# Performance work log

Measured on AMD Instinct MI355X. Metric: run time of the kernel, lower is better.

The kernel has to match this reference:

```python
import jax, jax.numpy as jnp
import numpy as np

NEG, NEG2, EPS, K = 0.01, 0.2, 1e-5, 10
B, N = 8, 2048

def lrelu(x, s):
    return jnp.where(x >= 0, x, s * x)

def bn_eval(x, g, b):
    # BatchNorm in eval mode with running_mean=0, running_var=1
    shp = [1] * x.ndim; shp[1] = -1
    return x * (g / np.sqrt(1.0 + EPS)).reshape(shp) + b.reshape(shp)

def conv1d(x, W, b):  # x [B,C,N], W [O,C]
    return jnp.einsum('bcn,oc->bon', x, W) + b[None, :, None]

def conv2d_1x1(x, W, b):  # x [B,C,N,K], W [O,C]
    return jnp.einsum('bcnk,oc->bonk', x, W) + b[None, :, None, None]

def edge_feats(x, k):
    # x: [B, d, N] -> [B, 2d, N, k]
    xt = jnp.swapaxes(x, 1, 2)                                   # [B,N,d]
    dist = (-2.0 * jnp.einsum('bnd,bdm->bnm', xt, x)
            + jnp.sum(xt ** 2, axis=2, keepdims=True)
            + jnp.sum(x ** 2, axis=1, keepdims=True))            # [B,N,N]
    idx = jnp.argsort(dist, axis=2)[:, :, 1:k + 1]               # [B,N,k]
    nbrs = jax.vmap(lambda xb, ib: xb[:, ib])(x, idx)            # [B,d,N,k]
    c = x[:, :, :, None]
    return jnp.concatenate([jnp.broadcast_to(c, nbrs.shape), nbrs - c], axis=1)

def edge_block(x, wc1, wcb1, bn1g, bn1b, wc2, wcb2, bn2g, bn2b,
               xc, xcb, xbng, xbnb, oW, ob):
    C = x.shape[1]
    ee = edge_feats(x, K)                                        # [B,2C,N,K]
    w = lrelu(bn_eval(conv2d_1x1(ee[:, C:], wc1, wcb1), bn1g, bn1b), NEG)
    w = lrelu(bn_eval(conv2d_1x1(w, wc2, wcb2), bn2g, bn2b), NEG)
    w = jax.nn.softmax(w, axis=-1)
    h = lrelu(bn_eval(conv2d_1x1(ee, xc, xcb), xbng, xbnb), NEG)
    # Conv2d(Fout, Fout, [1,K]): contract channels and neighbor axis
    return jnp.einsum('bcnj,ocj->bon', h * w, oW) + ob[None, :, None]

def adain(x, style, W, b):
    s = conv1d(style, W, b)
    g, be = jnp.split(s, 2, axis=1)
    m = jnp.mean(x, axis=2, keepdims=True)
    v = jnp.mean((x - m) ** 2, axis=2, keepdims=True)
    return g * ((x - m) * jax.lax.rsqrt(v + EPS)) + be

def _forward(z, x, hW1, hb1, hW2, hb2,
             e1_wc1, e1_wcb1, e1_bn1g, e1_bn1b, e1_wc2, e1_wcb2, e1_bn2g, e1_bn2b,
             e1_xc, e1_xcb, e1_xbng, e1_xbnb, e1_oW, e1_ob, a1_W, a1_b,
             e2_wc1, e2_wcb1, e2_bn1g, e2_bn1b, e2_wc2, e2_wcb2, e2_bn2g, e2_bn2b,
             e2_xc, e2_xcb, e2_xbng, e2_xbnb, e2_oW, e2_ob, a2_W, a2_b,
             gW1, gb1, gbn1g, gbn1b, gW2, gb2, gbn2g, gbn2b,
             tW1, tb1, tW2, tb2, tW3, tb3):
    st = jnp.swapaxes(jnp.concatenate([x, z], axis=-1), 1, 2)    # [B,3+nz,N]
    st = lrelu(conv1d(st, hW1, hb1), NEG)
    st = lrelu(conv1d(st, hW2, hb2), NEG)                        # [B,128,N]
    pc = jnp.swapaxes(x, 1, 2)                                   # [B,3,N]
    x1 = edge_block(pc, e1_wc1, e1_wcb1, e1_bn1g, e1_bn1b, e1_wc2, e1_wcb2,
                    e1_bn2g, e1_bn2b, e1_xc, e1_xcb, e1_xbng, e1_xbnb, e1_oW, e1_ob)
    x1 = adain(lrelu(x1, NEG2), st, a1_W, a1_b)                  # [B,64,N]
    x2 = edge_block(x1, e2_wc1, e2_wcb1, e2_bn1g, e2_bn1b, e2_wc2, e2_wcb2,
                    e2_bn2g, e2_bn2b, e2_xc, e2_xcb, e2_xbng, e2_xbnb, e2_oW, e2_ob)
    x2 = adain(lrelu(x2, NEG2), st, a2_W, a2_b)                  # [B,128,N]
    fg = jnp.max(x2, axis=2)                                     # [B,128]
    fg = lrelu(bn_eval(fg @ gW1.T + gb1, gbn1g, gbn1b), NEG)
    fg = lrelu(bn_eval(fg @ gW2.T + gb2, gbn2g, gbn2b), NEG)     # [B,512]
    fg = jnp.broadcast_to(fg[:, :, None], (fg.shape[0], 512, x2.shape[2]))
    feat = jnp.concatenate([fg, x2], axis=1)                     # [B,640,N]
    t = lrelu(conv1d(feat, tW1, tb1), NEG)
    t = lrelu(conv1d(t, tW2, tb2), NEG)
    t = conv1d(t, tW3, tb3)
    return jnp.swapaxes(t, 1, 2)                                 # [B,N,3]

_PARAM_SPECS = [
    ('hW1', (128, 131)), ('hb1', (128,)), ('hW2', (128, 128)), ('hb2', (128,)),
    ('e1_wc1', (32, 3)), ('e1_wcb1', (32,)), ('e1_bn1g', (32,)), ('e1_bn1b', (32,)),
    ('e1_wc2', (64, 32)), ('e1_wcb2', (64,)), ('e1_bn2g', (64,)), ('e1_bn2b', (64,)),
    ('e1_xc', (64, 6)), ('e1_xcb', (64,)), ('e1_xbng', (64,)), ('e1_xbnb', (64,)),
    ('e1_oW', (64, 64, 10)), ('e1_ob', (64,)), ('a1_W', (128, 128)), ('a1_b', (128,)),
    ('e2_wc1', (64, 64)), ('e2_wcb1', (64,)), ('e2_bn1g', (64,)), ('e2_bn1b', (64,)),
    ('e2_wc2', (128, 64)), ('e2_wcb2', (128,)), ('e2_bn2g', (128,)), ('e2_bn2b', (128,)),
    ('e2_xc', (128, 128)), ('e2_xcb', (128,)), ('e2_xbng', (128,)), ('e2_xbnb', (128,)),
    ('e2_oW', (128, 128, 10)), ('e2_ob', (128,)), ('a2_W', (256, 128)), ('a2_b', (256,)),
    ('gW1', (128, 128)), ('gb1', (128,)), ('gbn1g', (128,)), ('gbn1b', (128,)),
    ('gW2', (512, 128)), ('gb2', (512,)), ('gbn2g', (512,)), ('gbn2b', (512,)),
    ('tW1', (256, 640)), ('tb1', (256,)), ('tW2', (64, 256)), ('tb2', (64,)),
    ('tW3', (3, 64)), ('tb3', (3,)),
]

def setup_inputs() -> dict:
    key = jax.random.key(0)
    d = {
        'z': jax.random.normal(jax.random.fold_in(key, 1000), (B, N, 128), jnp.float32),
        'x': jax.random.normal(jax.random.fold_in(key, 1001), (B, N, 3), jnp.float32),
    }
    for i, (nm, sh) in enumerate(_PARAM_SPECS):
        v = 0.1 * jax.random.normal(jax.random.fold_in(key, i), sh, jnp.float32)
        if nm.endswith('g'):  # batchnorm gammas around 1
            v = v + 1.0
        d[nm] = v
    return d

def reference(z, x, hW1, hb1, hW2, hb2,
              e1_wc1, e1_wcb1, e1_bn1g, e1_bn1b, e1_wc2, e1_wcb2, e1_bn2g, e1_bn2b,
              e1_xc, e1_xcb, e1_xbng, e1_xbnb, e1_oW, e1_ob, a1_W, a1_b,
              e2_wc1, e2_wcb1, e2_bn1g, e2_bn1b, e2_wc2, e2_wcb2, e2_bn2g, e2_bn2b,
              e2_xc, e2_xcb, e2_xbng, e2_xbnb, e2_oW, e2_ob, a2_W, a2_b,
              gW1, gb1, gbn1g, gbn1b, gW2, gb2, gbn2g, gbn2b,
              tW1, tb1, tW2, tb2, tW3, tb3):
    return _forward(z, x, hW1, hb1, hW2, hb2,
                    e1_wc1, e1_wcb1, e1_bn1g, e1_bn1b, e1_wc2, e1_wcb2, e1_bn2g, e1_bn2b,
                    e1_xc, e1_xcb, e1_xbng, e1_xbnb, e1_oW, e1_ob, a1_W, a1_b,
                    e2_wc1, e2_wcb1, e2_bn1g, e2_bn1b, e2_wc2, e2_wcb2, e2_bn2g, e2_bn2b,
                    e2_xc, e2_xcb, e2_xbng, e2_xbnb, e2_oW, e2_ob, a2_W, a2_b,
                    gW1, gb1, gbn1g, gbn1b, gW2, gb2, gbn2g, gbn2b,
                    tW1, tb1, tW2, tb2, tW3, tb3)
```

## Files before the change

### kernel.cpp

```cpp
#include <hip/hip_runtime.h>
#include <math.h>

#define NPTS 2048
#define BATCH 8
#define KNB 10
#define NT (NPTS*KNB)

static __device__ __forceinline__ float lrelu(float x, float s){ return x >= 0.f ? x : s*x; }
static __device__ __forceinline__ double lrelu_d(double x, double s){ return x >= 0.0 ? x : s*x; }

template<int TM, int TN>
__global__ __launch_bounds__(256) void gemm_bn(
    const float* __restrict__ In, int ldn, size_t inBS, int koff,
    const float* __restrict__ W, int wstride, int wcol0,
    const float* __restrict__ cb, const float* __restrict__ bng, const float* __restrict__ bnb,
    const float* __restrict__ addBO, int addM,
    float* __restrict__ Out, int ldo, size_t outBS,
    int C, int act, float neg, int bbase)
{
  constexpr int RM = TM/16, RN = TN/16;
  __shared__ float As[16][TM+4];
  __shared__ float Bs[16][TN+4];
  const int b = bbase + blockIdx.z;
  const float* in = In + (size_t)b*inBS;
  float* outp = Out + (size_t)b*outBS;
  const int m0 = blockIdx.y*TM, n0 = blockIdx.x*TN;
  const int t = threadIdx.x;
  const int tmv = t>>4, tnv = t&15;
  float acc[RM][RN] = {};
  for (int k0=0; k0<C; k0+=16){
    #pragma unroll
    for (int s=0;s<RM;s++){
      const int i = t + s*256;
      const int k = i&15, m = i>>4;
      As[k][m] = W[(size_t)(m0+m)*wstride + wcol0 + k0 + k];
    }
    #pragma unroll
    for (int s=0;s<RN;s++){
      const int i = t + s*256;
      const int n = i & (TN-1), kk2 = i / TN;
      Bs[kk2][n] = in[(size_t)(koff + k0 + kk2)*ldn + n0 + n];
    }
    __syncthreads();
    #pragma unroll
    for (int kk=0;kk<16;kk++){
      float av[RM], bv[RN];
      #pragma unroll
      for (int s=0;s<RM/4;s++){
        float4 v = *(const float4*)&As[kk][tmv*RM + s*4];
        av[s*4]=v.x; av[s*4+1]=v.y; av[s*4+2]=v.z; av[s*4+3]=v.w;
      }
      #pragma unroll
      for (int s=0;s<RN/4;s++){
        float4 v = *(const float4*)&Bs[kk][tnv*RN + s*4];
        bv[s*4]=v.x; bv[s*4+1]=v.y; bv[s*4+2]=v.z; bv[s*4+3]=v.w;
      }
      #pragma unroll
      for (int i2=0;i2<RM;i2++)
        #pragma unroll
        for (int j2=0;j2<RN;j2++) acc[i2][j2] += av[i2]*bv[j2];
    }
    __syncthreads();
  }
  const float rs = 1.f/sqrtf(1.f + 1e-5f);
  #pragma unroll
  for (int i2=0;i2<RM;i2++){
    const int gm = m0 + tmv*RM + i2;
    float addv = cb ? cb[gm] : 0.f;
    if (addBO) addv += addBO[b*addM + gm];
    float sc = 1.f, bs = 0.f;
    if (bng){ sc = bng[gm]*rs; bs = bnb[gm]; }
    float* orow = outp + (size_t)gm*ldo + n0 + tnv*RN;
    #pragma unroll
    for (int j4=0;j4<RN/4;j4++){
      float4 o;
      float vv[4];
      #pragma unroll
      for (int q=0;q<4;q++){
        float v = acc[i2][j4*4+q] + addv;
        if (bng) v = v*sc + bs;
        if (act) v = lrelu(v, neg);
        vv[q] = v;
      }
      o.x=vv[0]; o.y=vv[1]; o.z=vv[2]; o.w=vv[3];
      *(float4*)&orow[j4*4] = o;
    }
  }
}

__global__ __launch_bounds__(256) void conv_gemm_exact(
    const float* __restrict__ in, const float* __restrict__ W, int wstride, int wcol0,
    const float* __restrict__ bias,
    float* __restrict__ out, int C, int M, int act, float neg)
{
  __shared__ float As[16][68];
  __shared__ float Bs[16][68];
  const int b = blockIdx.z;
  const int m0 = blockIdx.y*64, n0 = blockIdx.x*64;
  const int t = threadIdx.x;
  const int tm = t>>4, tn = t&15;
  float acc[4][4] = {};
  for (int k0 = 0; k0 < C; k0 += 16){
    #pragma unroll
    for (int i=0;i<4;i++){
      const int ii = t + i*256;
      const int k = ii&15, m = ii>>4;
      const int gm = m0+m, gk = k0+k;
      As[k][m] = (gm<M && gk<C) ? W[(size_t)gm*wstride + wcol0 + gk] : 0.f;
    }
    #pragma unroll
    for (int i=0;i<4;i++){
      const int ii = t + i*256;
      const int n = ii&63, k = ii>>6;
      const int gk = k0+k;
      Bs[k][n] = (gk<C) ? in[((size_t)b*C+gk)*NPTS + n0+n] : 0.f;
    }
    __syncthreads();
    #pragma unroll
    for (int k=0;k<16;k++){
      #pragma unroll
      for (int i=0;i<4;i++){
        const float a = As[k][tm*4+i];
        #pragma unroll
        for (int j=0;j<4;j++){
          acc[i][j] = __fadd_rn(acc[i][j], __fmul_rn(a, Bs[k][tn*4+j]));
        }
      }
    }
    __syncthreads();
  }
  #pragma unroll
  for (int i=0;i<4;i++){
    const int gm = m0 + tm*4 + i;
    if (gm < M){
      const float bv = bias ? bias[gm] : 0.f;
      #pragma unroll
      for (int j=0;j<4;j++){
        float v = __fadd_rn(acc[i][j], bv);
        if (act) v = (v >= 0.f) ? v : __fmul_rn(neg, v);
        out[((size_t)b*M+gm)*NPTS + n0 + tn*4 + j] = v;
      }
    }
  }
}

__global__ __launch_bounds__(256) void head1_exact(
    const float* __restrict__ x, const float* __restrict__ z,
    const float* __restrict__ W, const float* __restrict__ bias,
    float* __restrict__ outh)
{
  __shared__ float As[16][68];
  __shared__ float Bs[16][68];
  const int b = blockIdx.z;
  const int m0 = blockIdx.y*64, n0 = blockIdx.x*64;
  const int t = threadIdx.x;
  const int tm = t>>4, tn = t&15;
  float acc[4][4] = {};
  for (int k0 = 0; k0 < 144; k0 += 16){
    #pragma unroll
    for (int i=0;i<4;i++){
      const int ii = t + i*256;
      const int k = ii&15, m = ii>>4;
      const int gk = k0+k;
      As[k][m] = (gk<131) ? W[(size_t)(m0+m)*131 + gk] : 0.f;
    }
    #pragma unroll
    for (int i=0;i<4;i++){
      const int ii = t + i*256;
      const int k = ii&15, nn = ii>>4;
      const int gk = k0+k, gn = n0+nn;
      float v = 0.f;
      if (gk < 3)        v = x[((size_t)b*NPTS+gn)*3   + gk];
      else if (gk < 131) v = z[((size_t)b*NPTS+gn)*128 + (gk-3)];
      Bs[k][nn] = v;
    }
    __syncthreads();
    #pragma unroll
    for (int k=0;k<16;k++){
      #pragma unroll
      for (int i=0;i<4;i++){
        const float a = As[k][tm*4+i];
        #pragma unroll
        for (int j=0;j<4;j++){
          acc[i][j] = __fadd_rn(acc[i][j], __fmul_rn(a, Bs[k][tn*4+j]));
        }
      }
    }
    __syncthreads();
  }
  #pragma unroll
  for (int i=0;i<4;i++){
    const int gm = m0 + tm*4 + i;
    #pragma unroll
    for (int j=0;j<4;j++){
      float v = __fadd_rn(acc[i][j], bias[gm]);
      v = (v >= 0.f) ? v : __fmul_rn(0.01f, v);
      outh[((size_t)b*128+gm)*NPTS + n0 + tn*4 + j] = v;
    }
  }
}

__global__ __launch_bounds__(256) void norms3_f32(const float* __restrict__ Xn, float* __restrict__ XN)
{
  const int q = blockIdx.x*256 + threadIdx.x;
  const float* p = Xn + (size_t)q*3;
  float s = __fmul_rn(p[0],p[0]);
  s = __fadd_rn(s, __fmul_rn(p[1],p[1]));
  s = __fadd_rn(s, __fmul_rn(p[2],p[2]));
  XN[q] = s;
}

__global__ __launch_bounds__(256) void knn_part3(
    const float* __restrict__ Xn, const float* __restrict__ XN,
    double* __restrict__ topd, int* __restrict__ topi)
{
  const int t = threadIdx.x;
  const int qloc = t & 31, part = t >> 5;
  const int q = blockIdx.x*32 + qloc;
  const int b = q >> 11, n = q & (NPTS-1);
  const float* xb = Xn + (size_t)b*NPTS*3;
  const float qx = xb[(size_t)n*3+0], qy = xb[(size_t)n*3+1], qz = xb[(size_t)n*3+2];
  const float qn = XN[q];
  float td[11]; int ti[11];
  #pragma unroll
  for (int r=0;r<11;r++){ td[r] = 3.4e38f; ti[r] = 0x7fffffff; }
  const int m0 = part*(NPTS/8);
  for (int mm=0; mm<NPTS/8; mm++){
    const int m = m0 + mm;
    float dot = __fmul_rn(qx, xb[(size_t)m*3+0]);
    dot = __fadd_rn(dot, __fmul_rn(qy, xb[(size_t)m*3+1]));
    dot = __fadd_rn(dot, __fmul_rn(qz, xb[(size_t)m*3+2]));
    float dist = __fmul_rn(-2.f, dot);
    dist = __fadd_rn(dist, qn);
    dist = __fadd_rn(dist, XN[b*NPTS + m]);
    if (dist < td[10]){
      td[10] = dist; ti[10] = m;
      #pragma unroll
      for (int p=10;p>0;p--){
        if (td[p] < td[p-1]){
          float tf=td[p]; td[p]=td[p-1]; td[p-1]=tf;
          int   tt=ti[p]; ti[p]=ti[p-1]; ti[p-1]=tt;
        }
      }
    }
  }
  const size_t base = ((size_t)q*8 + part)*11;
  #pragma unroll
  for (int r=0;r<11;r++){ topd[base+r] = (double)td[r]; topi[base+r] = ti[r]; }
}

__global__ __launch_bounds__(256) void knn_merge_kernel(
    const double* __restrict__ topd, const int* __restrict__ topi, int* __restrict__ idxout)
{
  const int q = blockIdx.x*256 + threadIdx.x;
  double td[11]; int ti[11];
  #pragma unroll
  for (int r=0;r<11;r++){ td[r] = 1.0e308; ti[r] = 0x7fffffff; }
  const size_t base = (size_t)q*88;
  for (int s=0; s<88; s++){
    const double d = topd[base+s];
    const int  im = topi[base+s];
    if (d < td[10] || (d == td[10] && im < ti[10])){
      td[10] = d; ti[10] = im;
      #pragma unroll
      for (int p=10;p>0;p--){
        const bool sw = (td[p] < td[p-1]) || (td[p] == td[p-1] && ti[p] < ti[p-1]);
        if (sw){
          double tf=td[p]; td[p]=td[p-1]; td[p-1]=tf;
          int    tt=ti[p]; ti[p]=ti[p-1]; ti[p-1]=tt;
        }
      }
    }
  }
  #pragma unroll
  for (int j=0;j<KNB;j++) idxout[(size_t)q*KNB + j] = ti[j+1];
}

__global__ __launch_bounds__(256) void norms64_f32(const float* __restrict__ Xn, float* __restrict__ XN)
{
  const int q = blockIdx.x*256 + threadIdx.x;
  const float4* p4 = (const float4*)(Xn + (size_t)q*64);
  float s0=0.f,s1=0.f,s2=0.f,s3=0.f;
  #pragma unroll
  for (int d4=0; d4<16; d4++){
    float4 v = p4[d4];
    s0 += v.x*v.x; s1 += v.y*v.y; s2 += v.z*v.z; s3 += v.w*v.w;
  }
  XN[q] = (s0+s1)+(s2+s3);
}

__global__ __launch_bounds__(256) void knn_coarse(
    const float* __restrict__ Xn, const float* __restrict__ XN,
    float* __restrict__ topf, int* __restrict__ topi)
{
  __shared__ float Cs[64][68];
  __shared__ float xns[64];
  const int t = threadIdx.x;
  const int tq = t>>3, p = t&7;
  const int q0 = blockIdx.x*32;
  const int b  = q0 >> 11;
  const int gq = q0 + tq;
  const int nloc = (q0 & (NPTS-1)) + tq;
  const float* xb = Xn + (size_t)b*NPTS*64;
  float qv[64];
  {
    const float4* p4 = (const float4*)(xb + (size_t)nloc*64);
    #pragma unroll
    for (int d4=0; d4<16; d4++){ float4 v = p4[d4]; qv[d4*4]=v.x; qv[d4*4+1]=v.y; qv[d4*4+2]=v.z; qv[d4*4+3]=v.w; }
  }
  const float qn = XN[gq];
  float td[16]; int ti[16];
  #pragma unroll
  for (int r=0;r<16;r++){ td[r] = 3.4e38f; ti[r] = 0x7fffffff; }

  for (int m0=0; m0<NPTS; m0+=64){
    __syncthreads();
    #pragma unroll
    for (int s=0;s<4;s++){
      const int i = t + s*256;
      const int row = i>>4, f4 = i&15;
      float4 v = *(const float4*)(xb + (size_t)(m0+row)*64 + f4*4);
      *(float4*)&Cs[row][f4*4] = v;
    }
    if (t < 64) xns[t] = XN[b*NPTS + m0 + t];
    __syncthreads();
    #pragma unroll
    for (int jj=0;jj<8;jj++){
      const int row = jj*8 + p;
      float d0=0.f,d1=0.f,d2=0.f,d3=0.f;
      #pragma unroll
      for (int k4=0;k4<16;k4++){
        float4 v = *(const float4*)&Cs[row][k4*4];
        d0 += qv[k4*4+0]*v.x; d1 += qv[k4*4+1]*v.y;
        d2 += qv[k4*4+2]*v.z; d3 += qv[k4*4+3]*v.w;
      }
      const float dist = qn - 2.f*((d0+d1)+(d2+d3)) + xns[row];
      const int m = m0 + row;
      if (dist < td[15]){
        td[15] = dist; ti[15] = m;
        #pragma unroll
        for (int pp=15;pp>0;pp--){
          if (td[pp] < td[pp-1]){
            float tf=td[pp]; td[pp]=td[pp-1]; td[pp-1]=tf;
            int   tt=ti[pp]; ti[pp]=ti[pp-1]; ti[pp-1]=tt;
          }
        }
      }
    }
  }
  const size_t base = ((size_t)gq*8 + p)*16;
  #pragma unroll
  for (int r=0;r<16;r++){ topf[base+r] = td[r]; topi[base+r] = ti[r]; }
}

__global__ __launch_bounds__(256) void norms64d(const double* __restrict__ Xn, double* __restrict__ XN)
{
  const int q = blockIdx.x*256 + threadIdx.x;
  const double* p = Xn + (size_t)q*64;
  double s = 0.0;
  #pragma unroll
  for (int d=0; d<64; d++) s += p[d]*p[d];
  XN[q] = s;
}

__global__ __launch_bounds__(256) void knn_refine(
    const float* __restrict__ topf, const int* __restrict__ topi,
    const double* __restrict__ Xd, const double* __restrict__ XNd,
    int* __restrict__ idxout)
{
  const int q = blockIdx.x*256 + threadIdx.x;
  const int b = q >> 11;
  float tf[16]; int ti[16];
  #pragma unroll
  for (int r=0;r<16;r++){ tf[r] = 3.4e38f; ti[r] = 0x7fffffff; }
  const size_t base = (size_t)q*128;
  for (int s=0; s<128; s++){
    const float d = topf[base+s];
    const int  im = topi[base+s];
    if (d < tf[15] || (d == tf[15] && im < ti[15])){
      tf[15] = d; ti[15] = im;
      #pragma unroll
      for (int p=15;p>0;p--){
        const bool sw = (tf[p] < tf[p-1]) || (tf[p] == tf[p-1] && ti[p] < ti[p-1]);
        if (sw){
          float a=tf[p]; tf[p]=tf[p-1]; tf[p-1]=a;
          int   c=ti[p]; ti[p]=ti[p-1]; ti[p-1]=c;
        }
      }
    }
  }
  double qv[64];
  {
    const double2* p2 = (const double2*)(Xd + (size_t)q*64);
    #pragma unroll
    for (int d2=0; d2<32; d2++){ double2 v = p2[d2]; qv[d2*2]=v.x; qv[d2*2+1]=v.y; }
  }
  const double qn = XNd[q];
  double dd[11]; int di[11];
  #pragma unroll
  for (int r=0;r<11;r++){ dd[r] = 1.0e308; di[r] = 0x7fffffff; }
  for (int s=0; s<16; s++){
    const int m = ti[s];
    const double2* c2 = (const double2*)(Xd + ((size_t)(b*NPTS + m))*64);
    double d0=0.0,d1=0.0,d2s=0.0,d3=0.0;
    #pragma unroll
    for (int d4=0; d4<16; d4++){
      double2 va = c2[d4*2], vb = c2[d4*2+1];
      d0 += qv[d4*4+0]*va.x; d1 += qv[d4*4+1]*va.y;
      d2s+= qv[d4*4+2]*vb.x; d3 += qv[d4*4+3]*vb.y;
    }
    const double dot = (d0+d1)+(d2s+d3);
    const double dist = (qn - 2.0*dot) + XNd[b*NPTS + m];
    if (dist < dd[10] || (dist == dd[10] && m < di[10])){
      dd[10] = dist; di[10] = m;
      #pragma unroll
      for (int p=10;p>0;p--){
        const bool sw = (dd[p] < dd[p-1]) || (dd[p] == dd[p-1] && di[p] < di[p-1]);
        if (sw){
          double a=dd[p]; dd[p]=dd[p-1]; dd[p-1]=a;
          int    c=di[p]; di[p]=di[p-1]; di[p-1]=c;
        }
      }
    }
  }
  #pragma unroll
  for (int j=0;j<KNB;j++) idxout[(size_t)q*KNB + j] = di[j+1];
}

__global__ __launch_bounds__(512) void edge1_f64(
    const float* __restrict__ Xn, const int* __restrict__ idx,
    const float* __restrict__ wc1, const float* __restrict__ wcb1,
    const float* __restrict__ bn1g, const float* __restrict__ bn1b,
    const float* __restrict__ wc2, const float* __restrict__ wcb2,
    const float* __restrict__ bn2g, const float* __restrict__ bn2b,
    const float* __restrict__ xc,  const float* __restrict__ xcb,
    const float* __restrict__ xbng, const float* __restrict__ xbnb,
    const float* __restrict__ oWT, const float* __restrict__ ob,
    double* __restrict__ outX)
{
  __shared__ float wc1s[32][3];
  __shared__ float wc2s[64][33];
  __shared__ float xcs[64][7];
  __shared__ float wcb1s[32], wcb2s[64], xcbs[64];
  __shared__ double fs1d[32], fb1d[32], fs2d[64], fb2d[64], fsxd[64], fbxd[64];
  __shared__ float cenb[8][3], difb[8][3];
  __shared__ double w1bd[8][32];
  __shared__ float smw2[4096];
  __shared__ double hwbd[8][64];

  const int t = threadIdx.x;
  const double sq = sqrt(1.0 + 1e-5);
  for (int i=t; i<96;   i+=512) wc1s[i/3][i%3] = wc1[i];
  for (int i=t; i<2048; i+=512) wc2s[i/32][i%32] = wc2[i];
  for (int i=t; i<384;  i+=512) xcs[i/6][i%6] = xc[i];
  if (t < 32){ wcb1s[t]=wcb1[t]; fs1d[t]=(double)bn1g[t]/sq; fb1d[t]=(double)bn1b[t]; }
  else if (t < 96){ int o=t-32; wcb2s[o]=wcb2[o]; fs2d[o]=(double)bn2g[o]/sq; fb2d[o]=(double)bn2b[o]; }
  else if (t < 160){ int o=t-96; xcbs[o]=xcb[o]; fsxd[o]=(double)xbng[o]/sq; fbxd[o]=(double)xbnb[o]; }
  __syncthreads();

  const int wid = t>>6, lane = t&63;
  const int p = blockIdx.x*8 + wid;
  const int b = p >> 11, n = p & (NPTS-1);
  const float* xb = Xn + (size_t)b*NPTS*3;
  if (lane < 3) cenb[wid][lane] = xb[(size_t)n*3 + lane];
  __builtin_amdgcn_wave_barrier();
  const int* ip = idx + ((size_t)b*NPTS + n)*KNB;

  double w2r[KNB], hr[KNB];
  #pragma unroll
  for (int j=0;j<KNB;j++){
    const int id = ip[j];
    if (lane < 3) difb[wid][lane] = __fadd_rn(xb[(size_t)id*3 + lane], -cenb[wid][lane]);
    __builtin_amdgcn_wave_barrier();
    if (lane < 32){
      float s = __fmul_rn(wc1s[lane][0], difb[wid][0]);
      s = __fadd_rn(s, __fmul_rn(wc1s[lane][1], difb[wid][1]));
      s = __fadd_rn(s, __fmul_rn(wc1s[lane][2], difb[wid][2]));
      s = __fadd_rn(s, wcb1s[lane]);
      const double y = (double)s * fs1d[lane] + fb1d[lane];
      w1bd[wid][lane] = lrelu_d(y, 0.01);
    }
    __builtin_amdgcn_wave_barrier();
    {
      const int o = lane;
      double s2 = 0.0;
      #pragma unroll 8
      for (int m=0;m<32;m++) s2 += (double)wc2s[o][m] * w1bd[wid][m];
      s2 += (double)wcb2s[o];
      w2r[j] = lrelu_d(s2*fs2d[o] + fb2d[o], 0.01);
      float s3 = __fmul_rn(xcs[o][0], cenb[wid][0]);
      s3 = __fadd_rn(s3, __fmul_rn(xcs[o][1], cenb[wid][1]));
      s3 = __fadd_rn(s3, __fmul_rn(xcs[o][2], cenb[wid][2]));
      s3 = __fadd_rn(s3, __fmul_rn(xcs[o][3], difb[wid][0]));
      s3 = __fadd_rn(s3, __fmul_rn(xcs[o][4], difb[wid][1]));
      s3 = __fadd_rn(s3, __fmul_rn(xcs[o][5], difb[wid][2]));
      s3 = __fadd_rn(s3, xcbs[o]);
      hr[j] = lrelu_d((double)s3*fsxd[o] + fbxd[o], 0.01);
    }
    __builtin_amdgcn_wave_barrier();
  }

  double hw[KNB];
  {
    double mx = w2r[0];
    #pragma unroll
    for (int j=1;j<KNB;j++) mx = fmax(mx, w2r[j]);
    double ssum = 0.0;
    #pragma unroll
    for (int j=0;j<KNB;j++){ const double e = exp(w2r[j]-mx); w2r[j]=e; ssum+=e; }
    #pragma unroll
    for (int j=0;j<KNB;j++) hw[j] = hr[j]*(w2r[j]/ssum);
  }

  double acc = 0.0;
  #pragma unroll
  for (int j=0;j<KNB;j++){
    __syncthreads();
    for (int i=t; i<4096; i+=512) smw2[i] = oWT[(size_t)j*4096 + i];
    hwbd[wid][lane] = hw[j];
    __syncthreads();
    double s = 0.0;
    #pragma unroll 8
    for (int c=0;c<64;c++) s += (double)smw2[c*64 + lane]*hwbd[wid][c];
    acc += s;
  }
  outX[((size_t)b*64+lane)*NPTS + n] = acc + (double)ob[lane];
}

template<int CH>
__global__ void owt_kernel(const float* __restrict__ oW, float* __restrict__ oWT)
{
  const int i = blockIdx.x*256 + threadIdx.x;
  if (i < CH*CH*KNB){
    const int j  = i % KNB;
    const int c2 = (i / KNB) % CH;
    const int o  = i / (KNB*CH);
    oWT[((size_t)j*CH + c2)*CH + o] = oW[i];
  }
}

__global__ __launch_bounds__(256) void adain1_f64(
    double* __restrict__ X, const float* __restrict__ S)
{
  const int c = blockIdx.x, b = blockIdx.y;
  const int t = threadIdx.x;
  const size_t base = ((size_t)b*64 + c)*NPTS;
  __shared__ double red[256];
  double v[8];
  double s = 0.0;
  #pragma unroll
  for (int i=0;i<8;i++){
    double xv = X[base + t + i*256];
    xv = lrelu_d(xv, 0.2);
    v[i] = xv; s += xv;
  }
  red[t] = s; __syncthreads();
  for (int st=128; st>0; st>>=1){ if (t<st) red[t] += red[t+st]; __syncthreads(); }
  const double mean = red[0]/(double)NPTS;
  __syncthreads();
  double s2 = 0.0;
  #pragma unroll
  for (int i=0;i<8;i++){ const double d = v[i]-mean; s2 += d*d; }
  red[t] = s2; __syncthreads();
  for (int st=128; st>0; st>>=1){ if (t<st) red[t] += red[t+st]; __syncthreads(); }
  const double var  = red[0]/(double)NPTS;
  const double rstd = 1.0/sqrt(var + 1e-5);
  const float* g  = S + ((size_t)b*128 + c)*NPTS;
  const float* be = S + ((size_t)b*128 + 64 + c)*NPTS;
  #pragma unroll
  for (int i=0;i<8;i++){
    const int n = t + i*256;
    X[base+n] = (double)g[n]*((v[i]-mean)*rstd) + (double)be[n];
  }
}

__global__ __launch_bounds__(256) void transpose_cast64(
    const double* __restrict__ in, double* __restrict__ outT,
    float* __restrict__ outTf, float* __restrict__ outC)
{
  __shared__ double tile[64][65];
  const int b = blockIdx.y, n0 = blockIdx.x*64;
  const int t = threadIdx.x;
  for (int i=t; i<4096; i+=256){
    const int n=i&63, c=i>>6;
    const double v = in[((size_t)b*64+c)*NPTS + n0+n];
    tile[c][n] = v;
    outC[((size_t)b*64+c)*NPTS + n0+n] = (float)v;
  }
  __syncthreads();
  for (int i=t; i<4096; i+=256){
    const int c=i&63, n=i>>6;
    const double v = tile[c][n];
    outT [((size_t)b*NPTS+n0+n)*64 + c] = v;
    outTf[((size_t)b*NPTS+n0+n)*64 + c] = (float)v;
  }
}

__global__ __launch_bounds__(256) void kernelP(
    const float* __restrict__ x1c, const float* __restrict__ wc1,
    const float* __restrict__ xc,
    float* __restrict__ WCC, float* __restrict__ HCC)
{
  __shared__ float As[16][68];
  __shared__ float Bs[16][132];
  const int b = blockIdx.z;
  const int y = blockIdx.y;
  const int n0 = blockIdx.x*128;
  const int t = threadIdx.x;
  const int tm = t>>4, tn = t&15;
  float acc[4][8] = {};
  for (int k0=0; k0<64; k0+=16){
    #pragma unroll
    for (int s=0;s<4;s++){
      const int i = t + s*256;
      const int k = i&15, m = i>>4;
      float w;
      if (y == 0) w = wc1[(size_t)m*64 + k0 + k];
      else {
        const int c = (y-1)*64 + m;
        w = xc[(size_t)c*128 + k0 + k] - xc[(size_t)c*128 + 64 + k0 + k];
      }
      As[k][m] = w;
    }
    #pragma unroll
    for (int s=0;s<8;s++){
      const int i = t + s*256;
      const int n = i&127, kk = i>>7;
      Bs[kk][n] = x1c[((size_t)b*64 + k0 + kk)*NPTS + n0 + n];
    }
    __syncthreads();
    #pragma unroll
    for (int k=0;k<16;k++){
      float4 a4 = *(const float4*)&As[k][tm*4];
      const float av[4] = {a4.x, a4.y, a4.z, a4.w};
      #pragma unroll
      for (int j=0;j<8;j++){
        const float bv = Bs[k][tn + j*16];
        #pragma unroll
        for (int i2=0;i2<4;i2++) acc[i2][j] += av[i2]*bv;
      }
    }
    __syncthreads();
  }
  #pragma unroll
  for (int i2=0;i2<4;i2++){
    const int m = tm*4 + i2;
    #pragma unroll
    for (int j=0;j<8;j++){
      const int n = n0 + tn + j*16;
      if (y == 0) WCC[((size_t)b*64 + m)*NPTS + n] = acc[i2][j];
      else        HCC[((size_t)b*128 + (y-1)*64 + m)*NPTS + n] = acc[i2][j];
    }
  }
}

__global__ __launch_bounds__(256) void kernelA(
    const float* __restrict__ X1f, const int* __restrict__ IDX,
    const float* __restrict__ WCC,
    const float* __restrict__ wc1, const float* __restrict__ wcb1,
    const float* __restrict__ bn1g, const float* __restrict__ bn1b,
    float* __restrict__ W1, int bbase)
{
  __shared__ float wc1T[64*68];
  __shared__ float nbr[64*132];
  __shared__ int idx_l[128];
  const int b = bbase + blockIdx.z;
  const int n0 = blockIdx.x*128;
  const int t = threadIdx.x;
  const float* xb = X1f + (size_t)b*NPTS*64;

  if (t < 128){
    const int n = n0 + t;
    idx_l[t] = IDX[((size_t)b*NPTS + n/10)*KNB + (n%10)];
  }
  for (int i=t; i<4096; i+=256){
    const int k = i&63, m = i>>6;
    wc1T[k*68 + m] = wc1[(size_t)m*64 + k];
  }
  __syncthreads();
  const float4* xb4 = (const float4*)xb;
  #pragma unroll
  for (int r=0; r<8; r++){
    const int i = t + r*256;
    const int pos = i>>4, q4 = i&15;
    const float4 v = xb4[(size_t)idx_l[pos]*16 + q4];
    nbr[(q4*4+0)*132 + pos] = v.x;
    nbr[(q4*4+1)*132 + pos] = v.y;
    nbr[(q4*4+2)*132 + pos] = v.z;
    nbr[(q4*4+3)*132 + pos] = v.w;
  }
  __syncthreads();

  const int tm = t>>4, tn = t&15;
  float acc[4][8] = {};
  #pragma unroll 4
  for (int k=0;k<64;k++){
    float4 a4 = *(const float4*)&wc1T[k*68 + tm*4];
    const float av[4] = {a4.x, a4.y, a4.z, a4.w};
    #pragma unroll
    for (int j=0;j<8;j++){
      const float bv = nbr[k*132 + tn + j*16];
      #pragma unroll
      for (int i2=0;i2<4;i2++) acc[i2][j] += av[i2]*bv;
    }
  }
  const float rs = 1.f/sqrtf(1.f + 1e-5f);
  #pragma unroll
  for (int i2=0;i2<4;i2++){
    const int m = tm*4 + i2;
    const float bias = wcb1[m];
    const float sc = bn1g[m]*rs, bb = bn1b[m];
    #pragma unroll
    for (int j=0;j<8;j++){
      const int n = n0 + tn + j*16;
      const int p = n/10;
      float v = acc[i2][j] - WCC[((size_t)b*64 + m)*NPTS + p] + bias;
      v = lrelu(v*sc + bb, 0.01f);
      W1[((size_t)(b-bbase)*64 + m)*NT + n] = v;
    }
  }
}

#define C_WC2T 0
#define C_XCDT 4352
#define C_W1S  8704
#define C_NBRS 13952
#define C_TOT  19200
#define C_HW   0
#define C_OWL  5184

__global__ __launch_bounds__(256) void kernelC(
    const float* __restrict__ X1f, const int* __restrict__ IDX,
    const float* __restrict__ W1, const float* __restrict__ HCC,
    const float* __restrict__ wc2, const float* __restrict__ wcb2,
    const float* __restrict__ bn2g, const float* __restrict__ bn2b,
    const float* __restrict__ xc,  const float* __restrict__ xcb,
    const float* __restrict__ xbng, const float* __restrict__ xbnb,
    const float* __restrict__ oW, const float* __restrict__ ob,
    float* __restrict__ X2, int bbase)
{
  __shared__ float smC[C_TOT];
  __shared__ int idxC[80];
  const int b = bbase + blockIdx.z;
  const int n0 = blockIdx.x*80;
  const int p0 = n0/10;
  const int t = threadIdx.x;
  const float* xb = X1f + (size_t)b*NPTS*64;

  if (t < 80){
    const int n = n0 + t;
    idxC[t] = IDX[((size_t)b*NPTS + n/10)*KNB + (n%10)];
  }
  __syncthreads();

  const int tmv = t>>4, tnv = t&15, tnv5 = tnv*5;
  const int p_loc = tnv>>1, jh5 = (tnv&1)*5;
  const int o = t&127, phalf = t>>7;
  const float rs = 1.f/sqrtf(1.f + 1e-5f);
  float acc2[4] = {};

  for (int ch=0; ch<2; ch++){
    for (int i=t; i<4096; i+=256){
      const int k = i&63, cl = i>>6;
      smC[C_WC2T + k*68 + cl] = wc2[(size_t)(ch*64+cl)*64 + k];
      smC[C_XCDT + k*68 + cl] = xc[(size_t)(ch*64+cl)*128 + 64 + k];
    }
    for (int i=t; i<5120; i+=256){
      const int n = i%80, k = i/80;
      smC[C_W1S + k*82 + n] = W1[((size_t)(b-bbase)*64 + k)*NT + n0 + n];
    }
    {
      const float4* xb4 = (const float4*)xb;
      #pragma unroll
      for (int r=0;r<5;r++){
        const int i = t + r*256;
        const int pos = i>>4, q4 = i&15;
        const float4 v = xb4[(size_t)idxC[pos]*16 + q4];
        smC[C_NBRS + (q4*4+0)*82 + pos] = v.x;
        smC[C_NBRS + (q4*4+1)*82 + pos] = v.y;
        smC[C_NBRS + (q4*4+2)*82 + pos] = v.z;
        smC[C_NBRS + (q4*4+3)*82 + pos] = v.w;
      }
    }
    __syncthreads();

    float accw[4][5] = {}, acch[4][5] = {};
    #pragma unroll 2
    for (int k=0;k<64;k++){
      float4 a4 = *(const float4*)&smC[C_WC2T + k*68 + tmv*4];
      float4 x4 = *(const float4*)&smC[C_XCDT + k*68 + tmv*4];
      const float av[4] = {a4.x,a4.y,a4.z,a4.w};
      const float xv[4] = {x4.x,x4.y,x4.z,x4.w};
      float bw[5], bh[5];
      #pragma unroll
      for (int j=0;j<5;j++){
        bw[j] = smC[C_W1S  + k*82 + tnv5 + j];
        bh[j] = smC[C_NBRS + k*82 + tnv5 + j];
      }
      #pragma unroll
      for (int i2=0;i2<4;i2++)
        #pragma unroll
        for (int j=0;j<5;j++){ accw[i2][j]+=av[i2]*bw[j]; acch[i2][j]+=xv[i2]*bh[j]; }
    }

    float hwreg[4][5];
    #pragma unroll
    for (int i2=0;i2<4;i2++){
      const int c = ch*64 + tmv*4 + i2;
      const float s2 = bn2g[c]*rs, b2 = bn2b[c], cb2 = wcb2[c];
      const float sx = xbng[c]*rs, bx = xbnb[c], cbx = xcb[c];
      const float hcc = HCC[((size_t)b*128 + c)*NPTS + p0 + p_loc];
      float w2[5], hv[5];
      #pragma unroll
      for (int j=0;j<5;j++){
        w2[j] = lrelu((accw[i2][j] + cb2)*s2 + b2, 0.01f);
        hv[j] = lrelu((acch[i2][j] + hcc + cbx)*sx + bx, 0.01f);
      }
      float mx = w2[0];
      #pragma unroll
      for (int j=1;j<5;j++) mx = fmaxf(mx, w2[j]);
      mx = fmaxf(mx, __shfl_xor(mx, 1));
      float ssum = 0.f;
      #pragma unroll
      for (int j=0;j<5;j++){ w2[j] = expf(w2[j]-mx); ssum += w2[j]; }
      ssum += __shfl_xor(ssum, 1);
      const float inv = 1.f/ssum;
      #pragma unroll
      for (int j=0;j<5;j++) hwreg[i2][j] = hv[j]*(w2[j]*inv);
    }
    __syncthreads();

    #pragma unroll
    for (int i2=0;i2<4;i2++){
      const int cl = tmv*4 + i2;
      #pragma unroll
      for (int j=0;j<5;j++)
        smC[C_HW + p_loc*648 + cl*10 + jh5 + j] = hwreg[i2][j];
    }
    __syncthreads();

    for (int kc=0; kc<640; kc+=64){
      #pragma unroll
      for (int r=0;r<32;r++){
        const int i = t + r*256;
        const int oo = i>>6, kk = i&63;
        smC[C_OWL + oo*65 + kk] = oW[(size_t)oo*1280 + ch*640 + kc + kk];
      }
      __syncthreads();
      #pragma unroll 4
      for (int kk=0; kk<64; kk+=4){
        const float w0 = smC[C_OWL + o*65 + kk];
        const float w1v= smC[C_OWL + o*65 + kk+1];
        const float w2v= smC[C_OWL + o*65 + kk+2];
        const float w3v= smC[C_OWL + o*65 + kk+3];
        #pragma unroll
        for (int pp=0;pp<4;pp++){
          const float4 h4 = *(const float4*)&smC[C_HW + (phalf*4+pp)*648 + kc + kk];
          acc2[pp] += w0*h4.x + w1v*h4.y + w2v*h4.z + w3v*h4.w;
        }
      }
      __syncthreads();
    }
  }
  const float obv = ob[o];
  #pragma unroll
  for (int pp=0;pp<4;pp++)
    X2[((size_t)b*128 + o)*NPTS + p0 + phalf*4 + pp] = acc2[pp] + obv;
}

template<int CH>
__global__ __launch_bounds__(256) void adain_kernel(
    float* __restrict__ X, const float* __restrict__ S)
{
  const int c = blockIdx.x, b = blockIdx.y;
  const int t = threadIdx.x;
  const size_t base = ((size_t)b*CH + c)*NPTS;
  __shared__ float red[256];
  float v[8];
  float s = 0.f;
  #pragma unroll
  for (int i=0;i<8;i++){
    float xv = X[base + t + i*256];
    xv = lrelu(xv, 0.2f);
    v[i] = xv; s += xv;
  }
  red[t] = s; __syncthreads();
  for (int st=128; st>0; st>>=1){ if (t<st) red[t] += red[t+st]; __syncthreads(); }
  const float mean = red[0]*(1.f/NPTS);
  __syncthreads();
  float s2 = 0.f;
  #pragma unroll
  for (int i=0;i<8;i++){ const float d = v[i]-mean; s2 += d*d; }
  red[t] = s2; __syncthreads();
  for (int st=128; st>0; st>>=1){ if (t<st) red[t] += red[t+st]; __syncthreads(); }
  const float var  = red[0]*(1.f/NPTS);
  const float rstd = 1.f/sqrtf(var + 1e-5f);
  const float* g  = S + ((size_t)b*2*CH + c)*NPTS;
  const float* be = S + ((size_t)b*2*CH + CH + c)*NPTS;
  #pragma unroll
  for (int i=0;i<8;i++){
    const int n = t + i*256;
    X[base+n] = g[n]*((v[i]-mean)*rstd) + be[n];
  }
}

__global__ __launch_bounds__(256) void maxn_kernel(const float* __restrict__ X, float* __restrict__ FG)
{
  const int c = blockIdx.x, b = blockIdx.y;
  const int t = threadIdx.x;
  const float* p = X + ((size_t)b*128 + c)*NPTS;
  __shared__ float red[256];
  float m = -3.4e38f;
  for (int i=t; i<NPTS; i+=256) m = fmaxf(m, p[i]);
  red[t] = m; __syncthreads();
  for (int st=128; st>0; st>>=1){ if (t<st) red[t] = fmaxf(red[t], red[t+st]); __syncthreads(); }
  if (t == 0) FG[b*128+c] = red[0];
}

__global__ __launch_bounds__(512) void fc_kernel(
    const float* __restrict__ FG,
    const float* __restrict__ gW1, const float* __restrict__ gb1,
    const float* __restrict__ gbn1g, const float* __restrict__ gbn1b,
    const float* __restrict__ gW2, const float* __restrict__ gb2,
    const float* __restrict__ gbn2g, const float* __restrict__ gbn2b,
    const float* __restrict__ tW1, const float* __restrict__ tb1,
    float* __restrict__ FGP)
{
  const int b = blockIdx.x, t = threadIdx.x;
  __shared__ float fg[128], h1[128], h2[512];
  const float rs = 1.f/sqrtf(1.f + 1e-5f);
  if (t < 128) fg[t] = FG[b*128+t];
  __syncthreads();
  if (t < 128){
    float s = 0.f;
    for (int c=0;c<128;c++) s += gW1[t*128+c]*fg[c];
    s += gb1[t];
    s = s*(gbn1g[t]*rs) + gbn1b[t];
    h1[t] = lrelu(s, 0.01f);
  }
  __syncthreads();
  {
    float s = 0.f;
    for (int c=0;c<128;c++) s += gW2[t*128+c]*h1[c];
    s += gb2[t];
    s = s*(gbn2g[t]*rs) + gbn2b[t];
    h2[t] = lrelu(s, 0.01f);
  }
  __syncthreads();
  if (t < 256){
    float s = tb1[t];
    for (int c=0;c<512;c++) s += tW1[(size_t)t*640 + c]*h2[c];
    FGP[b*256+t] = s;
  }
}

__global__ __launch_bounds__(256) void t3_kernel(
    const float* __restrict__ T2, const float* __restrict__ tW3,
    const float* __restrict__ tb3, float* __restrict__ outp)
{
  __shared__ float w[192];
  const int t = threadIdx.x;
  if (t < 192) w[t] = tW3[t];
  __syncthreads();
  const int b = blockIdx.y;
  const int n = blockIdx.x*256 + t;
  float a0 = tb3[0], a1 = tb3[1], a2 = tb3[2];
  for (int c=0;c<64;c++){
    const float v = T2[((size_t)b*64+c)*NPTS + n];
    a0 += w[c]*v; a1 += w[64+c]*v; a2 += w[128+c]*v;
  }
  float* op = outp + ((size_t)b*NPTS + n)*3;
  op[0]=a0; op[1]=a1; op[2]=a2;
}

extern "C" void kernel_launch(void* const* d_in, const int* in_sizes, int n_in,
                              void* d_out, int out_size, void* d_ws, size_t ws_size,
                              hipStream_t stream)
{
  (void)in_sizes; (void)n_in; (void)out_size; (void)ws_size;
  const float* z    = (const float*)d_in[0];
  const float* x    = (const float*)d_in[1];
  const float* hW1  = (const float*)d_in[2];
  const float* hb1  = (const float*)d_in[3];
  const float* hW2  = (const float*)d_in[4];
  const float* hb2  = (const float*)d_in[5];
  const float* e1_wc1 = (const float*)d_in[6];
  const float* e1_wcb1= (const float*)d_in[7];
  const float* e1_bn1g= (const float*)d_in[8];
  const float* e1_bn1b= (const float*)d_in[9];
  const float* e1_wc2 = (const float*)d_in[10];
  const float* e1_wcb2= (const float*)d_in[11];
  const float* e1_bn2g= (const float*)d_in[12];
  const float* e1_bn2b= (const float*)d_in[13];
  const float* e1_xc  = (const float*)d_in[14];
  const float* e1_xcb = (const float*)d_in[15];
  const float* e1_xbng= (const float*)d_in[16];
  const float* e1_xbnb= (const float*)d_in[17];
  const float* e1_oW  = (const float*)d_in[18];
  const float* e1_ob  = (const float*)d_in[19];
  const float* a1_W   = (const float*)d_in[20];
  const float* a1_b   = (const float*)d_in[21];
  const float* e2_wc1 = (const float*)d_in[22];
  const float* e2_wcb1= (const float*)d_in[23];
  const float* e2_bn1g= (const float*)d_in[24];
  const float* e2_bn1b= (const float*)d_in[25];
  const float* e2_wc2 = (const float*)d_in[26];
  const float* e2_wcb2= (const float*)d_in[27];
  const float* e2_bn2g= (const float*)d_in[28];
  const float* e2_bn2b= (const float*)d_in[29];
  const float* e2_xc  = (const float*)d_in[30];
  const float* e2_xcb = (const float*)d_in[31];
  const float* e2_xbng= (const float*)d_in[32];
  const float* e2_xbnb= (const float*)d_in[33];
  const float* e2_oW  = (const float*)d_in[34];
  const float* e2_ob  = (const float*)d_in[35];
  const float* a2_W   = (const float*)d_in[36];
  const float* a2_b   = (const float*)d_in[37];
  const float* gW1    = (const float*)d_in[38];
  const float* gb1    = (const float*)d_in[39];
  const float* gbn1g  = (const float*)d_in[40];
  const float* gbn1b  = (const float*)d_in[41];
  const float* gW2    = (const float*)d_in[42];
  const float* gb2    = (const float*)d_in[43];
  const float* gbn2g  = (const float*)d_in[44];
  const float* gbn2b  = (const float*)d_in[45];
  const float* tW1    = (const float*)d_in[46];
  const float* tb1    = (const float*)d_in[47];
  const float* tW2    = (const float*)d_in[48];
  const float* tb2    = (const float*)d_in[49];
  const float* tW3    = (const float*)d_in[50];
  const float* tb3    = (const float*)d_in[51];
  float* out = (float*)d_out;
  float* ws  = (float*)d_ws;

  size_t off = 0;
  float*  ST    = ws + off; off += (size_t)BATCH*128*NPTS;
  float*  Sbuf  = ws + off; off += (size_t)BATCH*256*NPTS;
  float*  X1f   = ws + off; off += (size_t)BATCH*NPTS*64;
  float*  X2    = ws + off; off += (size_t)BATCH*128*NPTS;
  float*  T1    = ws + off; off += (size_t)BATCH*256*NPTS;
  float*  T2    = ws + off; off += (size_t)BATCH*64*NPTS;
  int*    IDX   = (int*)(ws + off); off += (size_t)BATCH*NPTS*KNB;
  float*  OW1T  = ws + off; off += (size_t)64*64*KNB;
  float*  XN3f  = ws + off; off += (size_t)BATCH*NPTS;
  double* XN64  = (double*)(ws + off); off += (size_t)2*BATCH*NPTS;
  float*  FG    = ws + off; off += (size_t)BATCH*128;
  float*  FGP   = ws + off; off += (size_t)BATCH*256;
  off = (off + 1) & ~(size_t)1;
  double* X1_64 = (double*)(ws + off); off += (size_t)2*BATCH*64*NPTS;
  double* X1T64 = (double*)(ws + off); off += (size_t)2*BATCH*NPTS*64;

  double* TOPD  = (double*)T1;
  int*    TOPI  = (int*)Sbuf;
  float*  TOPF  = (float*)X1_64;
  int*    TOPI2 = (int*)T1;
  float*  X1c   = Sbuf;
  float*  WCC   = Sbuf + 1048576;
  float*  HCC   = Sbuf + 2097152;
  float*  W1    = T1;

  owt_kernel<64><<<(64*64*KNB+255)/256, 256, 0, stream>>>(e1_oW, OW1T);

  head1_exact<<<dim3(32,2,8), 256, 0, stream>>>(x, z, hW1, hb1, T1);
  conv_gemm_exact<<<dim3(32,2,8), 256, 0, stream>>>(T1, hW2, 128, 0, hb2, ST, 128, 128, 1, 0.01f);

  norms3_f32<<<64, 256, 0, stream>>>(x, XN3f);
  knn_part3<<<512, 256, 0, stream>>>(x, XN3f, TOPD, TOPI);
  knn_merge_kernel<<<64, 256, 0, stream>>>(TOPD, TOPI, IDX);
  edge1_f64<<<2048, 512, 0, stream>>>(
      x, IDX, e1_wc1, e1_wcb1, e1_bn1g, e1_bn1b, e1_wc2, e1_wcb2, e1_bn2g, e1_bn2b,
      e1_xc, e1_xcb, e1_xbng, e1_xbnb, OW1T, e1_ob, X1_64);
  conv_gemm_exact<<<dim3(32,2,8), 256, 0, stream>>>(ST, a1_W, 128, 0, a1_b, Sbuf, 128, 128, 0, 0.f);
  adain1_f64<<<dim3(64,8), 256, 0, stream>>>(X1_64, Sbuf);

  transpose_cast64<<<dim3(32,8), 256, 0, stream>>>(X1_64, X1T64, X1f, X1c);

  norms64_f32<<<64, 256, 0, stream>>>(X1f, XN3f);
  norms64d<<<64, 256, 0, stream>>>(X1T64, XN64);
  knn_coarse<<<512, 256, 0, stream>>>(X1f, XN3f, TOPF, TOPI2);
  knn_refine<<<64, 256, 0, stream>>>(TOPF, TOPI2, X1T64, XN64, IDX);

  kernelP<<<dim3(16,3,8), 256, 0, stream>>>(X1c, e2_wc1, e2_xc, WCC, HCC);
  for (int lb=0; lb<4; lb++){
    const int bbase = lb*2;
    kernelA<<<dim3(NT/128,1,2), 256, 0, stream>>>(
        X1f, IDX, WCC, e2_wc1, e2_wcb1, e2_bn1g, e2_bn1b, W1, bbase);
    kernelC<<<dim3(NT/80,1,2), 256, 0, stream>>>(
        X1f, IDX, W1, HCC, e2_wc2, e2_wcb2, e2_bn2g, e2_bn2b,
        e2_xc, e2_xcb, e2_xbng, e2_xbnb, e2_oW, e2_ob, X2, bbase);
  }

  gemm_bn<128,128><<<dim3(NPTS/128,2,8), 256, 0, stream>>>(
      ST, NPTS, (size_t)128*NPTS, 0, a2_W, 128, 0, a2_b, nullptr, nullptr, nullptr, 0,
      Sbuf, NPTS, (size_t)256*NPTS, 128, 0, 0.f, 0);
  adain_kernel<128><<<dim3(128,8), 256, 0, stream>>>(X2, Sbuf);

  maxn_kernel<<<dim3(128,8), 256, 0, stream>>>(X2, FG);
  fc_kernel<<<8, 512, 0, stream>>>(FG, gW1, gb1, gbn1g, gbn1b, gW2, gb2, gbn2g, gbn2b, tW1, tb1, FGP);
  gemm_bn<128,128><<<dim3(NPTS/128,2,8), 256, 0, stream>>>(
      X2, NPTS, (size_t)128*NPTS, 0, tW1, 640, 512, nullptr, nullptr, nullptr, FGP, 256,
      T1, NPTS, (size_t)256*NPTS, 128, 1, 0.01f, 0);
  gemm_bn<64,128><<<dim3(NPTS/128,1,8), 256, 0, stream>>>(
      T1, NPTS, (size_t)256*NPTS, 0, tW2, 256, 0, tb2, nullptr, nullptr, nullptr, 0,
      T2, NPTS, (size_t)64*NPTS, 256, 1, 0.01f, 0);
  t3_kernel<<<dim3(8,8), 256, 0, stream>>>(T2, tW3, tb3, out);
}
```

Before: 1.579 ms.

## Keep edge1 weights in registers and reuse tiled gemm for exact convs

The first edge-conv kernel now loads its per-lane weight rows, biases and BN scales into registers and computes the neighbor differences per lane. This drops the shared-memory staging, the block-wide sync and most of the wave barriers. The separate exact conv GEMM is removed. The two head/style convolutions now run through the templated 128x128-tile gemm_bn with an EXACT mode that keeps round-to-nearest multiply and add without FMA contraction. This raises register pressure in edge1 (32 weight floats per lane) and launches far fewer blocks for the small convs, only 16 per batch.

```diff
diff --git a/kernel.cpp b/kernel.cpp
--- a/kernel.cpp
+++ b/kernel.cpp
@@ -9,7 +9,7 @@
 static __device__ __forceinline__ float lrelu(float x, float s){ return x >= 0.f ? x : s*x; }
 static __device__ __forceinline__ double lrelu_d(double x, double s){ return x >= 0.0 ? x : s*x; }
 
-template<int TM, int TN>
+template<int TM, int TN, bool EXACT=false>
 __global__ __launch_bounds__(256) void gemm_bn(
     const float* __restrict__ In, int ldn, size_t inBS, int koff,
     const float* __restrict__ W, int wstride, int wcol0,
@@ -58,7 +58,12 @@
       #pragma unroll
       for (int i2=0;i2<RM;i2++)
         #pragma unroll
-        for (int j2=0;j2<RN;j2++) acc[i2][j2] += av[i2]*bv[j2];
+        for (int j2=0;j2<RN;j2++){
+          if constexpr (EXACT)
+            acc[i2][j2] = __fadd_rn(acc[i2][j2], __fmul_rn(av[i2], bv[j2]));
+          else
+            acc[i2][j2] += av[i2]*bv[j2];
+        }
     }
     __syncthreads();
   }
@@ -77,69 +82,19 @@
       float vv[4];
       #pragma unroll
       for (int q=0;q<4;q++){
-        float v = acc[i2][j4*4+q] + addv;
-        if (bng) v = v*sc + bs;
-        if (act) v = lrelu(v, neg);
+        float v;
+        if constexpr (EXACT){
+          v = __fadd_rn(acc[i2][j4*4+q], addv);
+          if (act) v = (v >= 0.f) ? v : __fmul_rn(neg, v);
+        } else {
+          v = acc[i2][j4*4+q] + addv;
+          if (bng) v = v*sc + bs;
+          if (act) v = lrelu(v, neg);
+        }
         vv[q] = v;
       }
       o.x=vv[0]; o.y=vv[1]; o.z=vv[2]; o.w=vv[3];
       *(float4*)&orow[j4*4] = o;
-    }
-  }
-}
-
-__global__ __launch_bounds__(256) void conv_gemm_exact(
-    const float* __restrict__ in, const float* __restrict__ W, int wstride, int wcol0,
-    const float* __restrict__ bias,
-    float* __restrict__ out, int C, int M, int act, float neg)
-{
-  __shared__ float As[16][68];
-  __shared__ float Bs[16][68];
-  const int b = blockIdx.z;
-  const int m0 = blockIdx.y*64, n0 = blockIdx.x*64;
-  const int t = threadIdx.x;
-  const int tm = t>>4, tn = t&15;
-  float acc[4][4] = {};
-  for (int k0 = 0; k0 < C; k0 += 16){
-    #pragma unroll
-    for (int i=0;i<4;i++){
-      const int ii = t + i*256;
-      const int k = ii&15, m = ii>>4;
-      const int gm = m0+m, gk = k0+k;
-      As[k][m] = (gm<M && gk<C) ? W[(size_t)gm*wstride + wcol0 + gk] : 0.f;
-    }
-    #pragma unroll
-    for (int i=0;i<4;i++){
-      const int ii = t + i*256;
-      const int n = ii&63, k = ii>>6;
-      const int gk = k0+k;
-      Bs[k][n] = (gk<C) ? in[((size_t)b*C+gk)*NPTS + n0+n] : 0.f;
-    }
-    __syncthreads();
-    #pragma unroll
-    for (int k=0;k<16;k++){
-      #pragma unroll
-      for (int i=0;i<4;i++){
-        const float a = As[k][tm*4+i];
-        #pragma unroll
-        for (int j=0;j<4;j++){
-          acc[i][j] = __fadd_rn(acc[i][j], __fmul_rn(a, Bs[k][tn*4+j]));
-        }
-      }
-    }
-    __syncthreads();
-  }
-  #pragma unroll
-  for (int i=0;i<4;i++){
-    const int gm = m0 + tm*4 + i;
-    if (gm < M){
-      const float bv = bias ? bias[gm] : 0.f;
-      #pragma unroll
-      for (int j=0;j<4;j++){
-        float v = __fadd_rn(acc[i][j], bv);
-        if (act) v = (v >= 0.f) ? v : __fmul_rn(neg, v);
-        out[((size_t)b*M+gm)*NPTS + n0 + tn*4 + j] = v;
-      }
     }
   }
 }
@@ -438,64 +393,70 @@
     const float* __restrict__ oWT, const float* __restrict__ ob,
     double* __restrict__ outX)
 {
-  __shared__ float wc1s[32][3];
-  __shared__ float wc2s[64][33];
-  __shared__ float xcs[64][7];
-  __shared__ float wcb1s[32], wcb2s[64], xcbs[64];
-  __shared__ double fs1d[32], fb1d[32], fs2d[64], fb2d[64], fsxd[64], fbxd[64];
-  __shared__ float cenb[8][3], difb[8][3];
   __shared__ double w1bd[8][32];
   __shared__ float smw2[4096];
   __shared__ double hwbd[8][64];
 
   const int t = threadIdx.x;
+  const int wid = t>>6, lane = t&63;
   const double sq = sqrt(1.0 + 1e-5);
-  for (int i=t; i<96;   i+=512) wc1s[i/3][i%3] = wc1[i];
-  for (int i=t; i<2048; i+=512) wc2s[i/32][i%32] = wc2[i];
-  for (int i=t; i<384;  i+=512) xcs[i/6][i%6] = xc[i];
-  if (t < 32){ wcb1s[t]=wcb1[t]; fs1d[t]=(double)bn1g[t]/sq; fb1d[t]=(double)bn1b[t]; }
-  else if (t < 96){ int o=t-32; wcb2s[o]=wcb2[o]; fs2d[o]=(double)bn2g[o]/sq; fb2d[o]=(double)bn2b[o]; }
-  else if (t < 160){ int o=t-96; xcbs[o]=xcb[o]; fsxd[o]=(double)xbng[o]/sq; fbxd[o]=(double)xbnb[o]; }
-  __syncthreads();
-
-  const int wid = t>>6, lane = t&63;
+  const int m31 = lane & 31;
+
+  float wc1row[3];
+  wc1row[0] = wc1[m31*3+0]; wc1row[1] = wc1[m31*3+1]; wc1row[2] = wc1[m31*3+2];
+  const float wcb1r = wcb1[m31];
+  const double fs1r = (double)bn1g[m31]/sq, fb1r = (double)bn1b[m31];
+  float wc2row[32];
+  #pragma unroll
+  for (int m=0;m<32;m++) wc2row[m] = wc2[lane*32 + m];
+  const float wcb2r = wcb2[lane];
+  const double fs2r = (double)bn2g[lane]/sq, fb2r = (double)bn2b[lane];
+  float xcrow[6];
+  #pragma unroll
+  for (int c=0;c<6;c++) xcrow[c] = xc[lane*6 + c];
+  const float xcbr = xcb[lane];
+  const double fsxr = (double)xbng[lane]/sq, fbxr = (double)xbnb[lane];
+
   const int p = blockIdx.x*8 + wid;
   const int b = p >> 11, n = p & (NPTS-1);
   const float* xb = Xn + (size_t)b*NPTS*3;
-  if (lane < 3) cenb[wid][lane] = xb[(size_t)n*3 + lane];
-  __builtin_amdgcn_wave_barrier();
+  const float cen0 = xb[(size_t)n*3+0];
+  const float cen1 = xb[(size_t)n*3+1];
+  const float cen2 = xb[(size_t)n*3+2];
   const int* ip = idx + ((size_t)b*NPTS + n)*KNB;
 
   double w2r[KNB], hr[KNB];
   #pragma unroll
   for (int j=0;j<KNB;j++){
     const int id = ip[j];
-    if (lane < 3) difb[wid][lane] = __fadd_rn(xb[(size_t)id*3 + lane], -cenb[wid][lane]);
-    __builtin_amdgcn_wave_barrier();
-    if (lane < 32){
-      float s = __fmul_rn(wc1s[lane][0], difb[wid][0]);
-      s = __fadd_rn(s, __fmul_rn(wc1s[lane][1], difb[wid][1]));
-      s = __fadd_rn(s, __fmul_rn(wc1s[lane][2], difb[wid][2]));
-      s = __fadd_rn(s, wcb1s[lane]);
-      const double y = (double)s * fs1d[lane] + fb1d[lane];
-      w1bd[wid][lane] = lrelu_d(y, 0.01);
+    const float dif0 = __fadd_rn(xb[(size_t)id*3+0], -cen0);
+    const float dif1 = __fadd_rn(xb[(size_t)id*3+1], -cen1);
+    const float dif2 = __fadd_rn(xb[(size_t)id*3+2], -cen2);
+    {
+      float s = __fmul_rn(wc1row[0], dif0);
+      s = __fadd_rn(s, __fmul_rn(wc1row[1], dif1));
+      s = __fadd_rn(s, __fmul_rn(wc1row[2], dif2));
+      s = __fadd_rn(s, wcb1r);
+      const double w1v = lrelu_d((double)s * fs1r + fb1r, 0.01);
+      if (lane < 32) w1bd[wid][lane] = w1v;
     }
     __builtin_amdgcn_wave_barrier();
     {
-      const int o = lane;
       double s2 = 0.0;
       #pragma unroll 8
-      for (int m=0;m<32;m++) s2 += (double)wc2s[o][m] * w1bd[wid][m];
-      s2 += (double)wcb2s[o];
-      w2r[j] = lrelu_d(s2*fs2d[o] + fb2d[o], 0.01);
-      float s3 = __fmul_rn(xcs[o][0], cenb[wid][0]);
-      s3 = __fadd_rn(s3, __fmul_rn(xcs[o][1], cenb[wid][1]));
-      s3 = __fadd_rn(s3, __fmul_rn(xcs[o][2], cenb[wid][2]));
-      s3 = __fadd_rn(s3, __fmul_rn(xcs[o][3], difb[wid][0]));
-      s3 = __fadd_rn(s3, __fmul_rn(xcs[o][4], difb[wid][1]));
-      s3 = __fadd_rn(s3, __fmul_rn(xcs[o][5], difb[wid][2]));
-      s3 = __fadd_rn(s3, xcbs[o]);
-      hr[j] = lrelu_d((double)s3*fsxd[o] + fbxd[o], 0.01);
+      for (int m=0;m<32;m++) s2 += (double)wc2row[m] * w1bd[wid][m];
+      s2 += (double)wcb2r;
+      w2r[j] = lrelu_d(s2*fs2r + fb2r, 0.01);
+    }
+    {
+      float s3 = __fmul_rn(xcrow[0], cen0);
+      s3 = __fadd_rn(s3, __fmul_rn(xcrow[1], cen1));
+      s3 = __fadd_rn(s3, __fmul_rn(xcrow[2], cen2));
+      s3 = __fadd_rn(s3, __fmul_rn(xcrow[3], dif0));
+      s3 = __fadd_rn(s3, __fmul_rn(xcrow[4], dif1));
+      s3 = __fadd_rn(s3, __fmul_rn(xcrow[5], dif2));
+      s3 = __fadd_rn(s3, xcbr);
+      hr[j] = lrelu_d((double)s3*fsxr + fbxr, 0.01);
     }
     __builtin_amdgcn_wave_barrier();
   }
@@ -1062,7 +1023,9 @@
   owt_kernel<64><<<(64*64*KNB+255)/256, 256, 0, stream>>>(e1_oW, OW1T);
 
   head1_exact<<<dim3(32,2,8), 256, 0, stream>>>(x, z, hW1, hb1, T1);
-  conv_gemm_exact<<<dim3(32,2,8), 256, 0, stream>>>(T1, hW2, 128, 0, hb2, ST, 128, 128, 1, 0.01f);
+  gemm_bn<128,128,true><<<dim3(NPTS/128,1,8), 256, 0, stream>>>(
+      T1, NPTS, (size_t)128*NPTS, 0, hW2, 128, 0, hb2, nullptr, nullptr, nullptr, 0,
+      ST, NPTS, (size_t)128*NPTS, 128, 1, 0.01f, 0);
 
   norms3_f32<<<64, 256, 0, stream>>>(x, XN3f);
   knn_part3<<<512, 256, 0, stream>>>(x, XN3f, TOPD, TOPI);
@@ -1070,7 +1033,9 @@
   edge1_f64<<<2048, 512, 0, stream>>>(
       x, IDX, e1_wc1, e1_wcb1, e1_bn1g, e1_bn1b, e1_wc2, e1_wcb2, e1_bn2g, e1_bn2b,
       e1_xc, e1_xcb, e1_xbng, e1_xbnb, OW1T, e1_ob, X1_64);
-  conv_gemm_exact<<<dim3(32,2,8), 256, 0, stream>>>(ST, a1_W, 128, 0, a1_b, Sbuf, 128, 128, 0, 0.f);
+  gemm_bn<128,128,true><<<dim3(NPTS/128,1,8), 256, 0, stream>>>(
+      ST, NPTS, (size_t)128*NPTS, 0, a1_W, 128, 0, a1_b, nullptr, nullptr, nullptr, 0,
+      Sbuf, NPTS, (size_t)128*NPTS, 128, 0, 0.f, 0);
   adain1_f64<<<dim3(64,8), 256, 0, stream>>>(X1_64, Sbuf);
 
   transpose_cast64<<<dim3(32,8), 256, 0, stream>>>(X1_64, X1T64, X1f, X1c);
```

After: 1.558 ms, median of 2. About the same (-1.3%).
